# Kernel optimization log

Hardware: AMD Instinct MI355X
Metric: run time of the kernel (lower is better)

The kernel has to match this reference:

```python
import jax, jax.numpy as jnp
import numpy as np

EPS = 1e-8  # torch F.cosine_similarity default eps
NEG = -1e9  # masked_fill value


def setup_inputs() -> dict:
    key = jax.random.key(0)
    k1, k2, k3 = jax.random.split(key, 3)
    B, Sq, Sk, D = 4, 2048, 2048, 1024
    query = jax.random.normal(k1, (B, Sq, 1, D), dtype=jnp.float32)
    key_t = jax.random.normal(k2, (B, 1, Sk, D), dtype=jnp.float32)
    mask = jax.random.randint(k3, (B, Sk), 0, 2, dtype=jnp.int32)
    return {"query": query, "key": key_t, "mask": mask}


def reference(query, key, mask):
    # query: [B, Sq, 1, D], key: [B, 1, Sk, D]
    q = query[:, :, 0, :]  # [B, Sq, D]
    k = key[:, 0, :, :]    # [B, Sk, D]
    # cosine_similarity(q, k, dim=3) = (q.k) / (max(|q|,eps) * max(|k|,eps))
    qn = jnp.maximum(jnp.linalg.norm(q, axis=-1), EPS)  # [B, Sq]
    kn = jnp.maximum(jnp.linalg.norm(k, axis=-1), EPS)  # [B, Sk]
    dot = jnp.einsum('bqd,bkd->bqk', q, k)              # [B, Sq, Sk]
    scores = dot / (qn[:, :, None] * kn[:, None, :])
    # mask.unsqueeze(1).repeat(1, Sq, 1) -> broadcast [B, 1, Sk] over Sq
    scores = jnp.where(mask[:, None, :] == 0, NEG, scores)
    return scores
```

## Files before the change

kernel.cpp:

```cpp
#include <hip/hip_runtime.h>
#include <hip/hip_bf16.h>
#include <stdint.h>


constexpr int B_  = 4;
constexpr int SQ  = 2048;
constexpr int SK  = 2048;
constexpr int D_  = 1024;
constexpr int BM  = 128;
constexpr int BN  = 128;
constexpr int BK  = 64;

typedef __attribute__((ext_vector_type(8)))  short    short8;
typedef __attribute__((ext_vector_type(4)))  float    f32x4;
typedef __attribute__((ext_vector_type(16))) float    f32x16;
typedef __attribute__((ext_vector_type(4)))  unsigned uint4v;
typedef unsigned int u32;

__device__ inline unsigned pack_bf16(float lo, float hi) {
  union { float f; unsigned u; } a, b;
  a.f = lo; b.f = hi;
  return __builtin_amdgcn_perm(b.u, a.u, 0x07060302u);
}

__device__ inline void async_ld16(const void* g, void* l) {
  __builtin_amdgcn_global_load_lds((const __attribute__((address_space(1))) u32*)g,
                                   (__attribute__((address_space(3))) u32*)l, 16, 0, 0);
}

constexpr int ROWS_Q = B_ * SQ;
constexpr int ROWS_T = B_ * (SQ + SK);

__global__ __launch_bounds__(256) void convert_norm(
    const float* __restrict__ Q, const float* __restrict__ Km,
    unsigned short* __restrict__ Qb, unsigned short* __restrict__ Kb,
    float* __restrict__ invQ, float* __restrict__ invK)
{
  const int row  = blockIdx.x * 4 + (threadIdx.x >> 6);
  const int lane = threadIdx.x & 63;

  const float* src; unsigned short* dst; float* inv;
  if (row < ROWS_Q) {
    src = Q  + (size_t)row * D_;
    dst = Qb + (size_t)row * D_;
    inv = invQ + row;
  } else {
    int r = row - ROWS_Q;
    src = Km + (size_t)r * D_;
    dst = Kb + (size_t)r * D_;
    inv = invK + r;
  }

  const f32x4* s4 = (const f32x4*)(src + lane * 16);
  f32x4 v[4];
  #pragma unroll
  for (int i = 0; i < 4; ++i) v[i] = s4[i];

  float ss = 0.0f;
  unsigned p[8];
  #pragma unroll
  for (int i = 0; i < 4; ++i) {
    p[2*i]   = pack_bf16(v[i].x, v[i].y);
    p[2*i+1] = pack_bf16(v[i].z, v[i].w);
    ss += v[i].x*v[i].x + v[i].y*v[i].y + v[i].z*v[i].z + v[i].w*v[i].w;
  }
  uint4v w0 = {p[0], p[1], p[2], p[3]};
  uint4v w1 = {p[4], p[5], p[6], p[7]};
  uint4v* d4 = (uint4v*)(dst + lane * 16);
  d4[0] = w0; d4[1] = w1;

  #pragma unroll
  for (int off = 32; off > 0; off >>= 1) ss += __shfl_xor(ss, off);
  if (lane == 0) *inv = 1.0f / fmaxf(sqrtf(ss), 1e-8f);
}

__global__ __launch_bounds__(256, 4) void ca_gemm_bf(
    const unsigned short* __restrict__ Qb,
    const unsigned short* __restrict__ Kb,
    const float* __restrict__ invQ,
    const float* __restrict__ invK,
    const int*   __restrict__ mask,
    float*       __restrict__ out)
{
  __shared__ __align__(16) unsigned short As[BM * BK];
  __shared__ __align__(16) unsigned short Bs[BN * BK];

  const int tid  = threadIdx.x;
  const int lane = tid & 63;
  const int w    = tid >> 6;

  const int lid = blockIdx.x;
  const int xcd = lid & 7;
  const int idx = lid >> 3;
  const int sq  = xcd * 2 + (idx >> 6);
  const int b   = sq >> 2;
  const int qd  = sq & 3;
  const int ty  = (qd >> 1) * 8 + ((idx >> 3) & 7);
  const int tx  = (qd & 1) * 8 + (idx & 7);
  const int tm0 = ty * BM;
  const int tn0 = tx * BN;

  const int srow   = lane >> 3;
  const int gchunk = (lane & 7) ^ srow;

  const char* qrow = (const char*)(Qb + ((size_t)b * SQ + tm0 + w * 32 + srow) * D_) + gchunk * 16;
  const char* krow = (const char*)(Kb + ((size_t)b * SK + tn0 + w * 32 + srow) * D_) + gchunk * 16;
  const size_t rstep8 = (size_t)8 * D_ * 2;

  unsigned short* ldsA = &As[(size_t)(w * 32) * BK];
  unsigned short* ldsB = &Bs[(size_t)(w * 32) * BK];

  f32x16 acc[2][2];
  #pragma unroll
  for (int i = 0; i < 2; ++i)
    #pragma unroll
    for (int j = 0; j < 2; ++j)
      #pragma unroll
      for (int r = 0; r < 16; ++r) acc[i][j][r] = 0.0f;

  const int wm = (w >> 1) * 64;
  const int wn = (w & 1) * 64;
  const int ln = lane & 31;
  const int h  = lane >> 5;

  for (int k0 = 0; k0 < D_; k0 += BK) {
    __syncthreads();
    const size_t kb = (size_t)k0 * 2;
    #pragma unroll
    for (int i = 0; i < 4; ++i)
      async_ld16(qrow + kb + i * rstep8, ldsA + i * 8 * BK);
    #pragma unroll
    for (int i = 0; i < 4; ++i)
      async_ld16(krow + kb + i * rstep8, ldsB + i * 8 * BK);
    __syncthreads();

    #pragma unroll
    for (int s = 0; s < 4; ++s) {
      const int c = 2 * s + h;
      const int ra0 = wm + ln, ra1 = wm + 32 + ln;
      const int rb0 = wn + ln, rb1 = wn + 32 + ln;
      short8 a0 = *(const short8*)&As[(size_t)ra0 * BK + (size_t)((c ^ (ra0 & 7)) * 8)];
      short8 a1 = *(const short8*)&As[(size_t)ra1 * BK + (size_t)((c ^ (ra1 & 7)) * 8)];
      short8 b0 = *(const short8*)&Bs[(size_t)rb0 * BK + (size_t)((c ^ (rb0 & 7)) * 8)];
      short8 b1 = *(const short8*)&Bs[(size_t)rb1 * BK + (size_t)((c ^ (rb1 & 7)) * 8)];
      acc[0][0] = __builtin_amdgcn_mfma_f32_32x32x16_bf16(a0, b0, acc[0][0], 0, 0, 0);
      acc[0][1] = __builtin_amdgcn_mfma_f32_32x32x16_bf16(a0, b1, acc[0][1], 0, 0, 0);
      acc[1][0] = __builtin_amdgcn_mfma_f32_32x32x16_bf16(a1, b0, acc[1][0], 0, 0, 0);
      acc[1][1] = __builtin_amdgcn_mfma_f32_32x32x16_bf16(a1, b1, acc[1][1], 0, 0, 0);
    }
  }

  #pragma unroll
  for (int tj = 0; tj < 2; ++tj) {
    const int gc = tn0 + wn + tj * 32 + ln;
    const int mk = mask[b * SK + gc];
    const float ibv = invK[b * SK + gc];
    #pragma unroll
    for (int ti = 0; ti < 2; ++ti) {
      #pragma unroll
      for (int reg = 0; reg < 16; ++reg) {
        const int row = wm + ti * 32 + (reg & 3) + 8 * (reg >> 2) + 4 * h;
        const float iav = invQ[b * SQ + tm0 + row];
        float v = mk ? acc[ti][tj][reg] * iav * ibv : -1000000000.0f;
        out[((size_t)b * SQ + tm0 + row) * SK + gc] = v;
      }
    }
  }
}

constexpr int LDK = 40;

__global__ __launch_bounds__(256, 2) void ca_gemm(
    const float* __restrict__ Q, const float* __restrict__ Km,
    const int* __restrict__ mask, float* __restrict__ out)
{
  __shared__ __align__(16) short As[BM * LDK];
  __shared__ __align__(16) short Bs[BN * LDK];
  __shared__ float ssA_part[256];
  __shared__ float ssB_part[256];
  __shared__ float invA[BM];
  __shared__ float invB[BN];

  const int tid  = threadIdx.x;
  const int lane = tid & 63;
  const int w    = tid >> 6;
  const int b    = blockIdx.z;
  const int tm0  = blockIdx.y * BM;
  const int tn0  = blockIdx.x * BN;

  const int ra = tid >> 1;
  const int ka = (tid & 1) * 16;

  const float* qp = Q  + ((size_t)b * SQ + tm0 + ra) * D_ + ka;
  const float* kp = Km + ((size_t)b * SK + tn0 + ra) * D_ + ka;

  f32x4 zero4 = {0.0f, 0.0f, 0.0f, 0.0f};
  f32x4 acc[4][4];
  #pragma unroll
  for (int i = 0; i < 4; ++i)
    #pragma unroll
    for (int j = 0; j < 4; ++j) acc[i][j] = zero4;

  float ssA = 0.0f, ssB = 0.0f;

  const int wm = (w >> 1) * 64;
  const int wn = (w & 1) * 64;
  const int lr = lane & 15;
  const int lq = lane >> 4;

  short* aw = &As[ra * LDK + ka];
  short* bw = &Bs[ra * LDK + ka];

  for (int k0 = 0; k0 < D_; k0 += 32) {
    f32x4 av[4], bv[4];
    #pragma unroll
    for (int i = 0; i < 4; ++i) av[i] = *(const f32x4*)(qp + 4 * i);
    #pragma unroll
    for (int i = 0; i < 4; ++i) bv[i] = *(const f32x4*)(kp + 4 * i);
    qp += 32; kp += 32;

    unsigned pa[8], pb[8];
    #pragma unroll
    for (int i = 0; i < 4; ++i) {
      pa[2*i]   = pack_bf16(av[i].x, av[i].y);
      pa[2*i+1] = pack_bf16(av[i].z, av[i].w);
      pb[2*i]   = pack_bf16(bv[i].x, bv[i].y);
      pb[2*i+1] = pack_bf16(bv[i].z, bv[i].w);
      ssA += av[i].x*av[i].x + av[i].y*av[i].y + av[i].z*av[i].z + av[i].w*av[i].w;
      ssB += bv[i].x*bv[i].x + bv[i].y*bv[i].y + bv[i].z*bv[i].z + bv[i].w*bv[i].w;
    }

    __syncthreads();
    {
      uint4v wa0 = {pa[0], pa[1], pa[2], pa[3]};
      uint4v wa1 = {pa[4], pa[5], pa[6], pa[7]};
      uint4v wb0 = {pb[0], pb[1], pb[2], pb[3]};
      uint4v wb1 = {pb[4], pb[5], pb[6], pb[7]};
      *(uint4v*)(aw)     = wa0;
      *(uint4v*)(aw + 8) = wa1;
      *(uint4v*)(bw)     = wb0;
      *(uint4v*)(bw + 8) = wb1;
    }
    __syncthreads();

    short8 af[4], bf[4];
    #pragma unroll
    for (int t = 0; t < 4; ++t)
      af[t] = *(const short8*)&As[(wm + t * 16 + lr) * LDK + lq * 8];
    #pragma unroll
    for (int t = 0; t < 4; ++t)
      bf[t] = *(const short8*)&Bs[(wn + t * 16 + lr) * LDK + lq * 8];

    #pragma unroll
    for (int i = 0; i < 4; ++i)
      #pragma unroll
      for (int j = 0; j < 4; ++j)
        acc[i][j] = __builtin_amdgcn_mfma_f32_16x16x32_bf16(af[i], bf[j], acc[i][j], 0, 0, 0);
  }

  ssA_part[tid] = ssA;
  ssB_part[tid] = ssB;
  __syncthreads();
  if (tid < BM) {
    float s = ssA_part[2 * tid] + ssA_part[2 * tid + 1];
    invA[tid] = 1.0f / fmaxf(sqrtf(s), 1e-8f);
  } else {
    int r = tid - BM;
    float s = ssB_part[2 * r] + ssB_part[2 * r + 1];
    invB[r] = 1.0f / fmaxf(sqrtf(s), 1e-8f);
  }
  __syncthreads();

  #pragma unroll
  for (int tn = 0; tn < 4; ++tn) {
    const int lc = wn + tn * 16 + lr;
    const int gc = tn0 + lc;
    const int mk = mask[b * SK + gc];
    const float ibv = invB[lc];
    #pragma unroll
    for (int tm = 0; tm < 4; ++tm) {
      const int lrow = wm + tm * 16 + lq * 4;
      #pragma unroll
      for (int r = 0; r < 4; ++r) {
        float v = mk ? acc[tm][tn][r] * invA[lrow + r] * ibv : -1000000000.0f;
        out[((size_t)b * SQ + tm0 + lrow + r) * SK + gc] = v;
      }
    }
  }
}

extern "C" void kernel_launch(void* const* d_in, const int* in_sizes, int n_in,
                              void* d_out, int out_size, void* d_ws, size_t ws_size,
                              hipStream_t stream) {
  const float* Q    = (const float*)d_in[0];
  const float* Km   = (const float*)d_in[1];
  const int*   mask = (const int*)d_in[2];
  float*       out  = (float*)d_out;

  const size_t nQ   = (size_t)B_ * SQ * D_;
  const size_t nK   = (size_t)B_ * SK * D_;
  const size_t need = (nQ + nK) * 2 + (size_t)B_ * (SQ + SK) * 4;
  if (ws_size >= need) {
    unsigned short* Qb = (unsigned short*)d_ws;
    unsigned short* Kb = Qb + nQ;
    float*          iQ = (float*)(Kb + nK);
    float*          iK = iQ + (size_t)B_ * SQ;
    convert_norm<<<ROWS_T / 4, 256, 0, stream>>>(Q, Km, Qb, Kb, iQ, iK);
    ca_gemm_bf<<<dim3(1024), dim3(256), 0, stream>>>(Qb, Kb, iQ, iK, mask, out);
  } else {
    dim3 grid(SK / BN, SQ / BM, B_);
    ca_gemm<<<grid, dim3(256), 0, stream>>>(Q, Km, mask, out);
  }
}
```

Measured before the change: 158.4 us.

## Compact unmasked key columns and skip GEMM tiles for masked keys

Adds a per-batch mask scan that builds compacted lists of kept and masked key column indices. Only the kept key rows are converted to bf16, the GEMM launches tiles only over kept columns and scatters results through the index list, and a separate kernel writes the -1e9 fill into masked columns. With a random mask about half the key columns are masked, so roughly half the matmul work can be skipped. The cost is two extra launches, a serial scan done by a single wave per batch, and scattered rather than contiguous output stores.

```diff
diff --git a/kernel.cpp b/kernel.cpp
--- a/kernel.cpp
+++ b/kernel.cpp
@@ -28,13 +28,45 @@
                                    (__attribute__((address_space(3))) u32*)l, 16, 0, 0);
 }
 
+__global__ __launch_bounds__(64) void mask_scan(
+    const int* __restrict__ mask,
+    int* __restrict__ kept, int* __restrict__ cidx, int* __restrict__ mcol)
+{
+  const int b    = blockIdx.x;
+  const int lane = threadIdx.x;
+  const int* m   = mask + b * SK;
+  const int base = lane * 32;
+
+  int cnt1 = 0;
+  #pragma unroll
+  for (int i = 0; i < 32; ++i) cnt1 += (m[base + i] != 0);
+  int cnt0 = 32 - cnt1;
+
+  int p1 = cnt1, p0 = cnt0;
+  #pragma unroll
+  for (int off = 1; off < 64; off <<= 1) {
+    int t1 = __shfl_up(p1, off);
+    int t0 = __shfl_up(p0, off);
+    if (lane >= off) { p1 += t1; p0 += t0; }
+  }
+  int e1 = p1 - cnt1, e0 = p0 - cnt0;
+
+  for (int i = 0; i < 32; ++i) {
+    int k = base + i;
+    if (m[k] != 0) cidx[b * SK + e1++] = k;
+    else           mcol[b * SK + e0++] = k;
+  }
+  if (lane == 63) kept[b] = p1;
+}
+
 constexpr int ROWS_Q = B_ * SQ;
 constexpr int ROWS_T = B_ * (SQ + SK);
 
 __global__ __launch_bounds__(256) void convert_norm(
     const float* __restrict__ Q, const float* __restrict__ Km,
     unsigned short* __restrict__ Qb, unsigned short* __restrict__ Kb,
-    float* __restrict__ invQ, float* __restrict__ invK)
+    float* __restrict__ invQ, float* __restrict__ invK,
+    const int* __restrict__ kept, const int* __restrict__ cidx)
 {
   const int row  = blockIdx.x * 4 + (threadIdx.x >> 6);
   const int lane = threadIdx.x & 63;
@@ -45,8 +77,11 @@
     dst = Qb + (size_t)row * D_;
     inv = invQ + row;
   } else {
-    int r = row - ROWS_Q;
-    src = Km + (size_t)r * D_;
+    const int r = row - ROWS_Q;
+    const int b = r >> 11;
+    const int j = r & (SK - 1);
+    if (j >= kept[b]) return;
+    src = Km + ((size_t)b * SK + cidx[r]) * D_;
     dst = Kb + (size_t)r * D_;
     inv = invK + r;
   }
@@ -72,6 +107,20 @@
   #pragma unroll
   for (int off = 32; off > 0; off >>= 1) ss += __shfl_xor(ss, off);
   if (lane == 0) *inv = 1.0f / fmaxf(sqrtf(ss), 1e-8f);
+}
+
+__global__ __launch_bounds__(256) void fill_neg(
+    float* __restrict__ out, const int* __restrict__ kept, const int* __restrict__ mcol)
+{
+  const int blk  = blockIdx.x;
+  const int b    = blk >> 9;
+  const int q    = (blk & 511) * 4 + (threadIdx.x >> 6);
+  const int lane = threadIdx.x & 63;
+  const int nm   = SK - kept[b];
+  float* orow    = out + ((size_t)b * SQ + q) * SK;
+  const int* mc  = mcol + b * SK;
+  for (int j = lane; j < nm; j += 64)
+    orow[mc[j]] = -1000000000.0f;
 }
 
 __global__ __launch_bounds__(256, 4) void ca_gemm_bf(
@@ -79,7 +128,8 @@
     const unsigned short* __restrict__ Kb,
     const float* __restrict__ invQ,
     const float* __restrict__ invK,
-    const int*   __restrict__ mask,
+    const int*   __restrict__ kept,
+    const int*   __restrict__ cidx,
     float*       __restrict__ out)
 {
   __shared__ __align__(16) unsigned short As[BM * BK];
@@ -99,6 +149,9 @@
   const int tx  = (qd & 1) * 8 + (idx & 7);
   const int tm0 = ty * BM;
   const int tn0 = tx * BN;
+
+  const int keptb = kept[b];
+  if (tn0 >= keptb) return;
 
   const int srow   = lane >> 3;
   const int gchunk = (lane & 7) ^ srow;
@@ -152,17 +205,18 @@
 
   #pragma unroll
   for (int tj = 0; tj < 2; ++tj) {
-    const int gc = tn0 + wn + tj * 32 + ln;
-    const int mk = mask[b * SK + gc];
-    const float ibv = invK[b * SK + gc];
+    const int jcol  = tn0 + wn + tj * 32 + ln;
+    const bool valid = jcol < keptb;
+    const int gc    = cidx[b * SK + (valid ? jcol : 0)];
+    const float ibv = invK[b * SK + jcol];
     #pragma unroll
     for (int ti = 0; ti < 2; ++ti) {
       #pragma unroll
       for (int reg = 0; reg < 16; ++reg) {
         const int row = wm + ti * 32 + (reg & 3) + 8 * (reg >> 2) + 4 * h;
         const float iav = invQ[b * SQ + tm0 + row];
-        float v = mk ? acc[ti][tj][reg] * iav * ibv : -1000000000.0f;
-        out[((size_t)b * SQ + tm0 + row) * SK + gc] = v;
+        if (valid)
+          out[((size_t)b * SQ + tm0 + row) * SK + gc] = acc[ti][tj][reg] * iav * ibv;
       }
     }
   }
@@ -299,14 +353,22 @@
 
   const size_t nQ   = (size_t)B_ * SQ * D_;
   const size_t nK   = (size_t)B_ * SK * D_;
-  const size_t need = (nQ + nK) * 2 + (size_t)B_ * (SQ + SK) * 4;
+  const size_t nInv = (size_t)B_ * (SQ + SK);
+  const size_t nIdx = (size_t)B_ * SK;
+  const size_t need = (nQ + nK) * 2 + nInv * 4 + 4 * 4 + nIdx * 4 * 2;
   if (ws_size >= need) {
     unsigned short* Qb = (unsigned short*)d_ws;
     unsigned short* Kb = Qb + nQ;
     float*          iQ = (float*)(Kb + nK);
     float*          iK = iQ + (size_t)B_ * SQ;
-    convert_norm<<<ROWS_T / 4, 256, 0, stream>>>(Q, Km, Qb, Kb, iQ, iK);
-    ca_gemm_bf<<<dim3(1024), dim3(256), 0, stream>>>(Qb, Kb, iQ, iK, mask, out);
+    int*          kept = (int*)(iK + (size_t)B_ * SK);
+    int*          cidx = kept + 4;
+    int*          mcol = cidx + nIdx;
+
+    mask_scan<<<B_, 64, 0, stream>>>(mask, kept, cidx, mcol);
+    convert_norm<<<ROWS_T / 4, 256, 0, stream>>>(Q, Km, Qb, Kb, iQ, iK, kept, cidx);
+    fill_neg<<<B_ * 512, 256, 0, stream>>>(out, kept, mcol);
+    ca_gemm_bf<<<dim3(1024), dim3(256), 0, stream>>>(Qb, Kb, iQ, iK, kept, cidx, out);
   } else {
     dim3 grid(SK / BN, SQ / BM, B_);
     ca_gemm<<<grid, dim3(256), 0, stream>>>(Q, Km, mask, out);
```

After: 207.0 us. 30.7% more time.

## Use 8-wave blocks with 32-wide K slices and per-wave 32x64 tiles

Applied to the files above, without the earlier changes.

The bf16 MFMA GEMM now launches 512 threads per block instead of 256. Each wave computes a 32x64 sub-tile instead of 64x64. The K slice shrinks from 64 to 32, so each thread issues a single 16-byte async LDS load per operand per iteration, with a matching XOR swizzle and precomputed LDS offsets. The goal is more resident waves to hide latency and less LDS per block. The cost is twice as many barrier-separated K iterations, less register reuse of A/B fragments per wave, and a stricter launch-bounds occupancy target that could force register spills.

```diff
diff --git a/kernel.cpp b/kernel.cpp
--- a/kernel.cpp
+++ b/kernel.cpp
@@ -9,7 +9,7 @@
 constexpr int D_  = 1024;
 constexpr int BM  = 128;
 constexpr int BN  = 128;
-constexpr int BK  = 64;
+constexpr int BK3 = 32;
 
 typedef __attribute__((ext_vector_type(8)))  short    short8;
 typedef __attribute__((ext_vector_type(4)))  float    f32x4;
@@ -74,7 +74,7 @@
   if (lane == 0) *inv = 1.0f / fmaxf(sqrtf(ss), 1e-8f);
 }
 
-__global__ __launch_bounds__(256, 4) void ca_gemm_bf(
+__global__ __launch_bounds__(512, 8) void ca_gemm_bf(
     const unsigned short* __restrict__ Qb,
     const unsigned short* __restrict__ Kb,
     const float* __restrict__ invQ,
@@ -82,8 +82,8 @@
     const int*   __restrict__ mask,
     float*       __restrict__ out)
 {
-  __shared__ __align__(16) unsigned short As[BM * BK];
-  __shared__ __align__(16) unsigned short Bs[BN * BK];
+  __shared__ __align__(16) unsigned short As[BM * BK3];
+  __shared__ __align__(16) unsigned short Bs[BN * BK3];
 
   const int tid  = threadIdx.x;
   const int lane = tid & 63;
@@ -100,53 +100,50 @@
   const int tm0 = ty * BM;
   const int tn0 = tx * BN;
 
-  const int srow   = lane >> 3;
-  const int gchunk = (lane & 7) ^ srow;
-
-  const char* qrow = (const char*)(Qb + ((size_t)b * SQ + tm0 + w * 32 + srow) * D_) + gchunk * 16;
-  const char* krow = (const char*)(Kb + ((size_t)b * SK + tn0 + w * 32 + srow) * D_) + gchunk * 16;
-  const size_t rstep8 = (size_t)8 * D_ * 2;
-
-  unsigned short* ldsA = &As[(size_t)(w * 32) * BK];
-  unsigned short* ldsB = &Bs[(size_t)(w * 32) * BK];
-
-  f32x16 acc[2][2];
-  #pragma unroll
-  for (int i = 0; i < 2; ++i)
-    #pragma unroll
-    for (int j = 0; j < 2; ++j)
-      #pragma unroll
-      for (int r = 0; r < 16; ++r) acc[i][j][r] = 0.0f;
-
-  const int wm = (w >> 1) * 64;
+  const int g = (tid & 3) ^ ((tid >> 3) & 3);
+  const char* qs = (const char*)(Qb + ((size_t)b * SQ + tm0 + (tid >> 2)) * D_) + g * 16;
+  const char* ks = (const char*)(Kb + ((size_t)b * SK + tn0 + (tid >> 2)) * D_) + g * 16;
+  unsigned short* dA = As + tid * 8;
+  unsigned short* dB = Bs + tid * 8;
+
+  f32x16 acc[2];
+  #pragma unroll
+  for (int n = 0; n < 2; ++n)
+    #pragma unroll
+    for (int r = 0; r < 16; ++r) acc[n][r] = 0.0f;
+
+  const int wm = (w >> 1) * 32;
   const int wn = (w & 1) * 64;
   const int ln = lane & 31;
   const int h  = lane >> 5;
-
-  for (int k0 = 0; k0 < D_; k0 += BK) {
+  const int ra  = wm + ln;
+  const int rb0 = wn + ln;
+  const int rb1 = wn + 32 + ln;
+
+  int offA[2], offB0[2], offB1[2];
+  #pragma unroll
+  for (int s = 0; s < 2; ++s) {
+    const int c = 2 * s + h;
+    offA[s]  = ra  * BK3 + ((c ^ ((ra  >> 1) & 3)) * 8);
+    offB0[s] = rb0 * BK3 + ((c ^ ((rb0 >> 1) & 3)) * 8);
+    offB1[s] = rb1 * BK3 + ((c ^ ((rb1 >> 1) & 3)) * 8);
+  }
+
+  for (int k0 = 0; k0 < D_; k0 += BK3) {
     __syncthreads();
-    const size_t kb = (size_t)k0 * 2;
-    #pragma unroll
-    for (int i = 0; i < 4; ++i)
-      async_ld16(qrow + kb + i * rstep8, ldsA + i * 8 * BK);
-    #pragma unroll
-    for (int i = 0; i < 4; ++i)
-      async_ld16(krow + kb + i * rstep8, ldsB + i * 8 * BK);
+    async_ld16(qs, dA);
+    async_ld16(ks, dB);
+    qs += BK3 * 2;
+    ks += BK3 * 2;
     __syncthreads();
 
     #pragma unroll
-    for (int s = 0; s < 4; ++s) {
-      const int c = 2 * s + h;
-      const int ra0 = wm + ln, ra1 = wm + 32 + ln;
-      const int rb0 = wn + ln, rb1 = wn + 32 + ln;
-      short8 a0 = *(const short8*)&As[(size_t)ra0 * BK + (size_t)((c ^ (ra0 & 7)) * 8)];
-      short8 a1 = *(const short8*)&As[(size_t)ra1 * BK + (size_t)((c ^ (ra1 & 7)) * 8)];
-      short8 b0 = *(const short8*)&Bs[(size_t)rb0 * BK + (size_t)((c ^ (rb0 & 7)) * 8)];
-      short8 b1 = *(const short8*)&Bs[(size_t)rb1 * BK + (size_t)((c ^ (rb1 & 7)) * 8)];
-      acc[0][0] = __builtin_amdgcn_mfma_f32_32x32x16_bf16(a0, b0, acc[0][0], 0, 0, 0);
-      acc[0][1] = __builtin_amdgcn_mfma_f32_32x32x16_bf16(a0, b1, acc[0][1], 0, 0, 0);
-      acc[1][0] = __builtin_amdgcn_mfma_f32_32x32x16_bf16(a1, b0, acc[1][0], 0, 0, 0);
-      acc[1][1] = __builtin_amdgcn_mfma_f32_32x32x16_bf16(a1, b1, acc[1][1], 0, 0, 0);
+    for (int s = 0; s < 2; ++s) {
+      short8 a0 = *(const short8*)&As[offA[s]];
+      short8 b0 = *(const short8*)&Bs[offB0[s]];
+      short8 b1 = *(const short8*)&Bs[offB1[s]];
+      acc[0] = __builtin_amdgcn_mfma_f32_32x32x16_bf16(a0, b0, acc[0], 0, 0, 0);
+      acc[1] = __builtin_amdgcn_mfma_f32_32x32x16_bf16(a0, b1, acc[1], 0, 0, 0);
     }
   }
 
@@ -156,14 +153,11 @@
     const int mk = mask[b * SK + gc];
     const float ibv = invK[b * SK + gc];
     #pragma unroll
-    for (int ti = 0; ti < 2; ++ti) {
-      #pragma unroll
-      for (int reg = 0; reg < 16; ++reg) {
-        const int row = wm + ti * 32 + (reg & 3) + 8 * (reg >> 2) + 4 * h;
-        const float iav = invQ[b * SQ + tm0 + row];
-        float v = mk ? acc[ti][tj][reg] * iav * ibv : -1000000000.0f;
-        out[((size_t)b * SQ + tm0 + row) * SK + gc] = v;
-      }
+    for (int reg = 0; reg < 16; ++reg) {
+      const int row = wm + (reg & 3) + 8 * (reg >> 2) + 4 * h;
+      const float iav = invQ[b * SQ + tm0 + row];
+      float v = mk ? acc[tj][reg] * iav * ibv : -1000000000.0f;
+      out[((size_t)b * SQ + tm0 + row) * SK + gc] = v;
     }
   }
 }
@@ -306,7 +300,7 @@
     float*          iQ = (float*)(Kb + nK);
     float*          iK = iQ + (size_t)B_ * SQ;
     convert_norm<<<ROWS_T / 4, 256, 0, stream>>>(Q, Km, Qb, Kb, iQ, iK);
-    ca_gemm_bf<<<dim3(1024), dim3(256), 0, stream>>>(Qb, Kb, iQ, iK, mask, out);
+    ca_gemm_bf<<<dim3(1024), dim3(512), 0, stream>>>(Qb, Kb, iQ, iK, mask, out);
   } else {
     dim3 grid(SK / BN, SQ / BM, B_);
     ca_gemm<<<grid, dim3(256), 0, stream>>>(Q, Km, mask, out);
```

Measured after the change: 162.3 us. 2.5% more time.

## Fuse bf16 conversion and norm computation into single GEMM kernel

Applied to the files above, without the earlier changes.

Removes the separate convert_norm pre-pass and the workspace bf16 copies. The GEMM now loads fp32 Q/K directly, packs them to bf16 into swizzled LDS and accumulates squared norms per row in registers, then reduces them with shuffles before the epilogue. This drops one launch and the write and re-read of the bf16 intermediates. In exchange, each tile re-reads fp32 data, twice the bytes of bf16, redundantly across the 16 tiles sharing a row, and loses the async global-to-LDS loads, so conversion ALU work sits on the critical path.

```diff
diff --git a/kernel.cpp b/kernel.cpp
--- a/kernel.cpp
+++ b/kernel.cpp
@@ -1,7 +1,6 @@
 #include <hip/hip_runtime.h>
 #include <hip/hip_bf16.h>
 #include <stdint.h>
-
 
 constexpr int B_  = 4;
 constexpr int SQ  = 2048;
@@ -23,67 +22,20 @@
   return __builtin_amdgcn_perm(b.u, a.u, 0x07060302u);
 }
 
-__device__ inline void async_ld16(const void* g, void* l) {
-  __builtin_amdgcn_global_load_lds((const __attribute__((address_space(1))) u32*)g,
-                                   (__attribute__((address_space(3))) u32*)l, 16, 0, 0);
-}
-
-constexpr int ROWS_Q = B_ * SQ;
-constexpr int ROWS_T = B_ * (SQ + SK);
-
-__global__ __launch_bounds__(256) void convert_norm(
-    const float* __restrict__ Q, const float* __restrict__ Km,
-    unsigned short* __restrict__ Qb, unsigned short* __restrict__ Kb,
-    float* __restrict__ invQ, float* __restrict__ invK)
-{
-  const int row  = blockIdx.x * 4 + (threadIdx.x >> 6);
-  const int lane = threadIdx.x & 63;
-
-  const float* src; unsigned short* dst; float* inv;
-  if (row < ROWS_Q) {
-    src = Q  + (size_t)row * D_;
-    dst = Qb + (size_t)row * D_;
-    inv = invQ + row;
-  } else {
-    int r = row - ROWS_Q;
-    src = Km + (size_t)r * D_;
-    dst = Kb + (size_t)r * D_;
-    inv = invK + r;
-  }
-
-  const f32x4* s4 = (const f32x4*)(src + lane * 16);
-  f32x4 v[4];
-  #pragma unroll
-  for (int i = 0; i < 4; ++i) v[i] = s4[i];
-
-  float ss = 0.0f;
-  unsigned p[8];
-  #pragma unroll
-  for (int i = 0; i < 4; ++i) {
-    p[2*i]   = pack_bf16(v[i].x, v[i].y);
-    p[2*i+1] = pack_bf16(v[i].z, v[i].w);
-    ss += v[i].x*v[i].x + v[i].y*v[i].y + v[i].z*v[i].z + v[i].w*v[i].w;
-  }
-  uint4v w0 = {p[0], p[1], p[2], p[3]};
-  uint4v w1 = {p[4], p[5], p[6], p[7]};
-  uint4v* d4 = (uint4v*)(dst + lane * 16);
-  d4[0] = w0; d4[1] = w1;
-
-  #pragma unroll
-  for (int off = 32; off > 0; off >>= 1) ss += __shfl_xor(ss, off);
-  if (lane == 0) *inv = 1.0f / fmaxf(sqrtf(ss), 1e-8f);
-}
-
-__global__ __launch_bounds__(256, 4) void ca_gemm_bf(
-    const unsigned short* __restrict__ Qb,
-    const unsigned short* __restrict__ Kb,
-    const float* __restrict__ invQ,
-    const float* __restrict__ invK,
+__device__ inline float dot4(f32x4 v) {
+  return v.x*v.x + v.y*v.y + v.z*v.z + v.w*v.w;
+}
+
+__global__ __launch_bounds__(256, 4) void ca_fused(
+    const float* __restrict__ Q,
+    const float* __restrict__ Km,
     const int*   __restrict__ mask,
     float*       __restrict__ out)
 {
   __shared__ __align__(16) unsigned short As[BM * BK];
   __shared__ __align__(16) unsigned short Bs[BN * BK];
+  __shared__ float invA[BM];
+  __shared__ float invB[BN];
 
   const int tid  = threadIdx.x;
   const int lane = tid & 63;
@@ -100,15 +52,18 @@
   const int tm0 = ty * BM;
   const int tn0 = tx * BN;
 
-  const int srow   = lane >> 3;
-  const int gchunk = (lane & 7) ^ srow;
-
-  const char* qrow = (const char*)(Qb + ((size_t)b * SQ + tm0 + w * 32 + srow) * D_) + gchunk * 16;
-  const char* krow = (const char*)(Kb + ((size_t)b * SK + tn0 + w * 32 + srow) * D_) + gchunk * 16;
-  const size_t rstep8 = (size_t)8 * D_ * 2;
-
-  unsigned short* ldsA = &As[(size_t)(w * 32) * BK];
-  unsigned short* ldsB = &Bs[(size_t)(w * 32) * BK];
+  const int rS = tid >> 2;
+  const int qt = tid & 3;
+  const float* qp0 = Q  + ((size_t)b * SQ + tm0 + rS     ) * D_ + qt * 16;
+  const float* qp1 = Q  + ((size_t)b * SQ + tm0 + rS + 64) * D_ + qt * 16;
+  const float* kp0 = Km + ((size_t)b * SK + tn0 + rS     ) * D_ + qt * 16;
+  const float* kp1 = Km + ((size_t)b * SK + tn0 + rS + 64) * D_ + qt * 16;
+  unsigned short* wA0 = &As[(size_t)rS * BK];
+  unsigned short* wA1 = &As[(size_t)(rS + 64) * BK];
+  unsigned short* wB0 = &Bs[(size_t)rS * BK];
+  unsigned short* wB1 = &Bs[(size_t)(rS + 64) * BK];
+  const int pc0 = ((2 * qt)     ^ (rS & 7)) * 8;
+  const int pc1 = ((2 * qt + 1) ^ (rS & 7)) * 8;
 
   f32x16 acc[2][2];
   #pragma unroll
@@ -117,6 +72,8 @@
     for (int j = 0; j < 2; ++j)
       #pragma unroll
       for (int r = 0; r < 16; ++r) acc[i][j][r] = 0.0f;
+
+  float sQ0 = 0.0f, sQ1 = 0.0f, sK0 = 0.0f, sK1 = 0.0f;
 
   const int wm = (w >> 1) * 64;
   const int wn = (w & 1) * 64;
@@ -124,14 +81,63 @@
   const int h  = lane >> 5;
 
   for (int k0 = 0; k0 < D_; k0 += BK) {
+    f32x4 a0v[4], a1v[4];
+    #pragma unroll
+    for (int i = 0; i < 4; ++i) a0v[i] = *(const f32x4*)(qp0 + 4 * i);
+    #pragma unroll
+    for (int i = 0; i < 4; ++i) a1v[i] = *(const f32x4*)(qp1 + 4 * i);
+    qp0 += BK; qp1 += BK;
+
     __syncthreads();
-    const size_t kb = (size_t)k0 * 2;
-    #pragma unroll
-    for (int i = 0; i < 4; ++i)
-      async_ld16(qrow + kb + i * rstep8, ldsA + i * 8 * BK);
-    #pragma unroll
-    for (int i = 0; i < 4; ++i)
-      async_ld16(krow + kb + i * rstep8, ldsB + i * 8 * BK);
+
+    {
+      unsigned p0[8], p1[8];
+      #pragma unroll
+      for (int i = 0; i < 4; ++i) {
+        p0[2*i]   = pack_bf16(a0v[i].x, a0v[i].y);
+        p0[2*i+1] = pack_bf16(a0v[i].z, a0v[i].w);
+        p1[2*i]   = pack_bf16(a1v[i].x, a1v[i].y);
+        p1[2*i+1] = pack_bf16(a1v[i].z, a1v[i].w);
+        sQ0 += dot4(a0v[i]);
+        sQ1 += dot4(a1v[i]);
+      }
+      uint4v u00 = {p0[0], p0[1], p0[2], p0[3]};
+      uint4v u01 = {p0[4], p0[5], p0[6], p0[7]};
+      uint4v u10 = {p1[0], p1[1], p1[2], p1[3]};
+      uint4v u11 = {p1[4], p1[5], p1[6], p1[7]};
+      *(uint4v*)(wA0 + pc0) = u00;
+      *(uint4v*)(wA0 + pc1) = u01;
+      *(uint4v*)(wA1 + pc0) = u10;
+      *(uint4v*)(wA1 + pc1) = u11;
+    }
+
+    {
+      f32x4 b0v[4], b1v[4];
+      #pragma unroll
+      for (int i = 0; i < 4; ++i) b0v[i] = *(const f32x4*)(kp0 + 4 * i);
+      #pragma unroll
+      for (int i = 0; i < 4; ++i) b1v[i] = *(const f32x4*)(kp1 + 4 * i);
+      kp0 += BK; kp1 += BK;
+      unsigned p0[8], p1[8];
+      #pragma unroll
+      for (int i = 0; i < 4; ++i) {
+        p0[2*i]   = pack_bf16(b0v[i].x, b0v[i].y);
+        p0[2*i+1] = pack_bf16(b0v[i].z, b0v[i].w);
+        p1[2*i]   = pack_bf16(b1v[i].x, b1v[i].y);
+        p1[2*i+1] = pack_bf16(b1v[i].z, b1v[i].w);
+        sK0 += dot4(b0v[i]);
+        sK1 += dot4(b1v[i]);
+      }
+      uint4v u00 = {p0[0], p0[1], p0[2], p0[3]};
+      uint4v u01 = {p0[4], p0[5], p0[6], p0[7]};
+      uint4v u10 = {p1[0], p1[1], p1[2], p1[3]};
+      uint4v u11 = {p1[4], p1[5], p1[6], p1[7]};
+      *(uint4v*)(wB0 + pc0) = u00;
+      *(uint4v*)(wB0 + pc1) = u01;
+      *(uint4v*)(wB1 + pc0) = u10;
+      *(uint4v*)(wB1 + pc1) = u11;
+    }
+
     __syncthreads();
 
     #pragma unroll
@@ -150,140 +156,35 @@
     }
   }
 
+  {
+    float t;
+    t = sQ0 + __shfl_xor(sQ0, 1); sQ0 = t + __shfl_xor(t, 2);
+    t = sQ1 + __shfl_xor(sQ1, 1); sQ1 = t + __shfl_xor(t, 2);
+    t = sK0 + __shfl_xor(sK0, 1); sK0 = t + __shfl_xor(t, 2);
+    t = sK1 + __shfl_xor(sK1, 1); sK1 = t + __shfl_xor(t, 2);
+    if (qt == 0) {
+      invA[rS]      = 1.0f / fmaxf(sqrtf(sQ0), 1e-8f);
+      invA[rS + 64] = 1.0f / fmaxf(sqrtf(sQ1), 1e-8f);
+      invB[rS]      = 1.0f / fmaxf(sqrtf(sK0), 1e-8f);
+      invB[rS + 64] = 1.0f / fmaxf(sqrtf(sK1), 1e-8f);
+    }
+  }
+  __syncthreads();
+
   #pragma unroll
   for (int tj = 0; tj < 2; ++tj) {
-    const int gc = tn0 + wn + tj * 32 + ln;
-    const int mk = mask[b * SK + gc];
-    const float ibv = invK[b * SK + gc];
-    #pragma unroll
-    for (int ti = 0; ti < 2; ++ti) {
-      #pragma unroll
-      for (int reg = 0; reg < 16; ++reg) {
-        const int row = wm + ti * 32 + (reg & 3) + 8 * (reg >> 2) + 4 * h;
-        const float iav = invQ[b * SQ + tm0 + row];
-        float v = mk ? acc[ti][tj][reg] * iav * ibv : -1000000000.0f;
-        out[((size_t)b * SQ + tm0 + row) * SK + gc] = v;
-      }
-    }
-  }
-}
-
-constexpr int LDK = 40;
-
-__global__ __launch_bounds__(256, 2) void ca_gemm(
-    const float* __restrict__ Q, const float* __restrict__ Km,
-    const int* __restrict__ mask, float* __restrict__ out)
-{
-  __shared__ __align__(16) short As[BM * LDK];
-  __shared__ __align__(16) short Bs[BN * LDK];
-  __shared__ float ssA_part[256];
-  __shared__ float ssB_part[256];
-  __shared__ float invA[BM];
-  __shared__ float invB[BN];
-
-  const int tid  = threadIdx.x;
-  const int lane = tid & 63;
-  const int w    = tid >> 6;
-  const int b    = blockIdx.z;
-  const int tm0  = blockIdx.y * BM;
-  const int tn0  = blockIdx.x * BN;
-
-  const int ra = tid >> 1;
-  const int ka = (tid & 1) * 16;
-
-  const float* qp = Q  + ((size_t)b * SQ + tm0 + ra) * D_ + ka;
-  const float* kp = Km + ((size_t)b * SK + tn0 + ra) * D_ + ka;
-
-  f32x4 zero4 = {0.0f, 0.0f, 0.0f, 0.0f};
-  f32x4 acc[4][4];
-  #pragma unroll
-  for (int i = 0; i < 4; ++i)
-    #pragma unroll
-    for (int j = 0; j < 4; ++j) acc[i][j] = zero4;
-
-  float ssA = 0.0f, ssB = 0.0f;
-
-  const int wm = (w >> 1) * 64;
-  const int wn = (w & 1) * 64;
-  const int lr = lane & 15;
-  const int lq = lane >> 4;
-
-  short* aw = &As[ra * LDK + ka];
-  short* bw = &Bs[ra * LDK + ka];
-
-  for (int k0 = 0; k0 < D_; k0 += 32) {
-    f32x4 av[4], bv[4];
-    #pragma unroll
-    for (int i = 0; i < 4; ++i) av[i] = *(const f32x4*)(qp + 4 * i);
-    #pragma unroll
-    for (int i = 0; i < 4; ++i) bv[i] = *(const f32x4*)(kp + 4 * i);
-    qp += 32; kp += 32;
-
-    unsigned pa[8], pb[8];
-    #pragma unroll
-    for (int i = 0; i < 4; ++i) {
-      pa[2*i]   = pack_bf16(av[i].x, av[i].y);
-      pa[2*i+1] = pack_bf16(av[i].z, av[i].w);
-      pb[2*i]   = pack_bf16(bv[i].x, bv[i].y);
-      pb[2*i+1] = pack_bf16(bv[i].z, bv[i].w);
-      ssA += av[i].x*av[i].x + av[i].y*av[i].y + av[i].z*av[i].z + av[i].w*av[i].w;
-      ssB += bv[i].x*bv[i].x + bv[i].y*bv[i].y + bv[i].z*bv[i].z + bv[i].w*bv[i].w;
-    }
-
-    __syncthreads();
-    {
-      uint4v wa0 = {pa[0], pa[1], pa[2], pa[3]};
-      uint4v wa1 = {pa[4], pa[5], pa[6], pa[7]};
-      uint4v wb0 = {pb[0], pb[1], pb[2], pb[3]};
-      uint4v wb1 = {pb[4], pb[5], pb[6], pb[7]};
-      *(uint4v*)(aw)     = wa0;
-      *(uint4v*)(aw + 8) = wa1;
-      *(uint4v*)(bw)     = wb0;
-      *(uint4v*)(bw + 8) = wb1;
-    }
-    __syncthreads();
-
-    short8 af[4], bf[4];
-    #pragma unroll
-    for (int t = 0; t < 4; ++t)
-      af[t] = *(const short8*)&As[(wm + t * 16 + lr) * LDK + lq * 8];
-    #pragma unroll
-    for (int t = 0; t < 4; ++t)
-      bf[t] = *(const short8*)&Bs[(wn + t * 16 + lr) * LDK + lq * 8];
-
-    #pragma unroll
-    for (int i = 0; i < 4; ++i)
-      #pragma unroll
-      for (int j = 0; j < 4; ++j)
-        acc[i][j] = __builtin_amdgcn_mfma_f32_16x16x32_bf16(af[i], bf[j], acc[i][j], 0, 0, 0);
-  }
-
-  ssA_part[tid] = ssA;
-  ssB_part[tid] = ssB;
-  __syncthreads();
-  if (tid < BM) {
-    float s = ssA_part[2 * tid] + ssA_part[2 * tid + 1];
-    invA[tid] = 1.0f / fmaxf(sqrtf(s), 1e-8f);
-  } else {
-    int r = tid - BM;
-    float s = ssB_part[2 * r] + ssB_part[2 * r + 1];
-    invB[r] = 1.0f / fmaxf(sqrtf(s), 1e-8f);
-  }
-  __syncthreads();
-
-  #pragma unroll
-  for (int tn = 0; tn < 4; ++tn) {
-    const int lc = wn + tn * 16 + lr;
+    const int lc = wn + tj * 32 + ln;
     const int gc = tn0 + lc;
     const int mk = mask[b * SK + gc];
     const float ibv = invB[lc];
     #pragma unroll
-    for (int tm = 0; tm < 4; ++tm) {
-      const int lrow = wm + tm * 16 + lq * 4;
-      #pragma unroll
-      for (int r = 0; r < 4; ++r) {
-        float v = mk ? acc[tm][tn][r] * invA[lrow + r] * ibv : -1000000000.0f;
-        out[((size_t)b * SQ + tm0 + lrow + r) * SK + gc] = v;
+    for (int ti = 0; ti < 2; ++ti) {
+      #pragma unroll
+      for (int reg = 0; reg < 16; ++reg) {
+        const int row = wm + ti * 32 + (reg & 3) + 8 * (reg >> 2) + 4 * h;
+        const float iav = invA[row];
+        float v = mk ? acc[ti][tj][reg] * iav * ibv : -1000000000.0f;
+        out[((size_t)b * SQ + tm0 + row) * SK + gc] = v;
       }
     }
   }
@@ -296,19 +197,7 @@
   const float* Km   = (const float*)d_in[1];
   const int*   mask = (const int*)d_in[2];
   float*       out  = (float*)d_out;
-
-  const size_t nQ   = (size_t)B_ * SQ * D_;
-  const size_t nK   = (size_t)B_ * SK * D_;
-  const size_t need = (nQ + nK) * 2 + (size_t)B_ * (SQ + SK) * 4;
-  if (ws_size >= need) {
-    unsigned short* Qb = (unsigned short*)d_ws;
-    unsigned short* Kb = Qb + nQ;
-    float*          iQ = (float*)(Kb + nK);
-    float*          iK = iQ + (size_t)B_ * SQ;
-    convert_norm<<<ROWS_T / 4, 256, 0, stream>>>(Q, Km, Qb, Kb, iQ, iK);
-    ca_gemm_bf<<<dim3(1024), dim3(256), 0, stream>>>(Qb, Kb, iQ, iK, mask, out);
-  } else {
-    dim3 grid(SK / BN, SQ / BM, B_);
-    ca_gemm<<<grid, dim3(256), 0, stream>>>(Q, Km, mask, out);
-  }
-}
+  (void)d_ws; (void)ws_size;
+
+  ca_fused<<<dim3(1024), dim3(256), 0, stream>>>(Q, Km, mask, out);
+}
```

Measured after the change: 200.8 us. 26.8% more time.
